# Kernel optimization log

Measured on AMD Instinct MI355X. Metric: run time of the kernel, lower is better.

Reference implementation:

```python
import jax, jax.numpy as jnp
import numpy as np

B, T, S, M = 512, 256, 32, 4  # groups, timesteps, state dim, measure dim


def setup_inputs() -> dict:
    key = jax.random.key(0)
    k = jax.random.split(key, 7)
    obs = jax.random.normal(k[0], (B, T, M), jnp.float32)
    # stable transition matrix: scaled orthogonal
    A = jax.random.normal(k[1], (S, S), jnp.float32)
    F = (0.95 * jnp.linalg.qr(A)[0]).astype(jnp.float32)
    # PSD process noise
    Aq = jax.random.normal(k[2], (S, S), jnp.float32)
    Q = (0.05 * (Aq @ Aq.T) / S + 0.01 * jnp.eye(S)).astype(jnp.float32)
    H = (jax.random.normal(k[3], (M, S), jnp.float32) / jnp.sqrt(S)).astype(jnp.float32)
    # PSD measurement noise
    Ar = jax.random.normal(k[4], (M, M), jnp.float32)
    R = ((Ar @ Ar.T) / M + 0.1 * jnp.eye(M)).astype(jnp.float32)
    init_mean = jax.random.normal(k[5], (B, S), jnp.float32)
    Ai = jax.random.normal(k[6], (B, S, S), jnp.float32)
    init_cov = (jnp.einsum('bij,bkj->bik', Ai, Ai) / S + 0.1 * jnp.eye(S)).astype(jnp.float32)
    return {'input': obs, 'F': F, 'Q': Q, 'H': H, 'R': R,
            'init_mean': init_mean, 'init_cov': init_cov}


def reference(input, F, Q, H, R, init_mean, init_cov):
    """One-step-ahead Kalman filter predictions.
    Returns (meas_means [T,B,M], meas_covs [T,B,M,M])."""

    def step(carry, y):
        m, P = carry  # m: [B,S], P: [B,S,S]
        # --- update with observation y (time t-1) ---
        PHt = jnp.einsum('bij,mj->bim', P, H)                    # [B,S,M]
        Smeas = jnp.einsum('ms,bsn->bmn', H, PHt) + R            # [B,M,M]
        # K = P H^T S^{-1}  (S symmetric)
        K = jnp.swapaxes(jnp.linalg.solve(Smeas, jnp.swapaxes(PHt, -1, -2)), -1, -2)  # [B,S,M]
        resid = y - m @ H.T                                      # [B,M]
        m_u = m + jnp.einsum('bsm,bm->bs', K, resid)
        # (I - K H) P ; note H P = PHt^T since P symmetric
        P_u = P - jnp.einsum('bsm,bim->bsi', K, PHt)
        # --- predict ---
        m_p = m_u @ F.T
        P_p = jnp.einsum('ij,bjk,lk->bil', F, P_u, F) + Q
        # --- measurement distribution ---
        mm = m_p @ H.T                                           # [B,M]
        mc = jnp.einsum('ms,bsi,ni->bmn', H, P_p, H) + R         # [B,M,M]
        return (m_p, P_p), (mm, mc)

    # t = 0: measurement of the initial state prediction
    mm0 = init_mean @ H.T
    mc0 = jnp.einsum('ms,bsi,ni->bmn', H, init_cov, H) + R
    obs_tm1 = jnp.swapaxes(input[:, :-1, :], 0, 1)               # [T-1,B,M]
    _, (mms, mcs) = jax.lax.scan(step, (init_mean, init_cov), obs_tm1)
    meas_means = jnp.concatenate([mm0[None], mms], axis=0)       # [T,B,M]
    meas_covs = jnp.concatenate([mc0[None], mcs], axis=0)        # [T,B,M,M]
    return meas_means, meas_covs
```

## Files before the change

kernel.cpp:

```cpp
#include <hip/hip_runtime.h>

#define BB 512
#define TT 256

typedef __attribute__((ext_vector_type(8)))  short bf8;
typedef __attribute__((ext_vector_type(4)))  short bf4;
typedef __attribute__((ext_vector_type(16))) float f16v;
typedef __attribute__((ext_vector_type(4)))  float f4v;

#define MFMA(a,b,c) __builtin_amdgcn_mfma_f32_32x32x16_bf16((a),(b),(c),0,0,0)

static __device__ __forceinline__ unsigned short f2bf_rne(float x) {
    unsigned u = __builtin_bit_cast(unsigned, x);
    return (unsigned short)((u + 0x7FFFu + ((u >> 16) & 1u)) >> 16);
}
static __device__ __forceinline__ float bf2f(unsigned short h) {
    unsigned u = ((unsigned)h) << 16;
    return __builtin_bit_cast(float, u);
}
static __device__ __forceinline__ void tsplit(float x, short& hi, short& lo) {
    unsigned u = __builtin_bit_cast(unsigned, x);
    hi = (short)(u >> 16);
    float hf = __builtin_bit_cast(float, u & 0xFFFF0000u);
    float l  = x - hf;
    lo = (short)(__builtin_bit_cast(unsigned, l) >> 16);
}
static __device__ __forceinline__ bf8 ld8(const unsigned short* p) {
    bf4 a = *(const bf4*)p;
    bf4 b = *(const bf4*)(p + 4);
    bf8 r;
    r[0]=a[0]; r[1]=a[1]; r[2]=a[2]; r[3]=a[3];
    r[4]=b[0]; r[5]=b[1]; r[6]=b[2]; r[7]=b[3];
    return r;
}

__global__ __launch_bounds__(64)
void kalman_v5(const float* __restrict__ obs,
               const float* __restrict__ Fg,
               const float* __restrict__ Qg,
               const float* __restrict__ Hg,
               const float* __restrict__ Rg,
               const float* __restrict__ im,
               const float* __restrict__ ic,
               float* __restrict__ out)
{
    __shared__ __align__(16) unsigned short sT1h[32*36], sT1l[32*36];
    __shared__ __align__(16) unsigned short sPNh[4*36],  sPNl[4*36];
    __shared__ __align__(16) float sFH[36*40];
    __shared__ __align__(16) float sm[32];
    __shared__ __align__(16) float sS[16];
    __shared__ __align__(16) float sRes4[4];

    const int lane = threadIdx.x;
    const int b    = blockIdx.x;
    const int c    = lane & 31;
    const int h    = lane >> 5;

    bf8 Fh[2], Fl[2], Hh[2], Hl[2];
    #pragma unroll
    for (int kk = 0; kk < 2; ++kk) {
        #pragma unroll
        for (int j = 0; j < 8; ++j) {
            int k = kk*16 + h*8 + j;
            float f = Fg[c*32 + k];
            unsigned short fh = f2bf_rne(f);
            Fh[kk][j] = (short)fh;
            Fl[kk][j] = (short)f2bf_rne(f - bf2f(fh));
            float hv = (c < 4) ? Hg[c*32 + k] : 0.f;
            unsigned short hh = f2bf_rne(hv);
            Hh[kk][j] = (short)hh;
            Hl[kk][j] = (short)f2bf_rne(hv - bf2f(hh));
        }
    }

    f16v Qc, P;
    #pragma unroll
    for (int reg = 0; reg < 16; ++reg) {
        int row = (reg & 3) + 8*(reg >> 2) + 4*h;
        Qc[reg] = Qg[row*32 + c];
        P[reg]  = ic[(size_t)b*1024 + row*32 + c];
    }
    float Rc[4] = {0.f, 0.f, 0.f, 0.f};
    if (c < 4) {
        #pragma unroll
        for (int m = 0; m < 4; ++m) Rc[m] = Rg[m*4 + c];
    }

    #pragma unroll
    for (int e = lane; e < 1024; e += 64) sFH[(e >> 5)*40 + (e & 31)] = Fg[e];
    #pragma unroll
    for (int e = lane; e < 128; e += 64) sFH[(32 + (e >> 5))*40 + (e & 31)] = Hg[e];
    if (lane < 32) sm[lane] = im[b*32 + lane];

    const float* dotrow = &sFH[(lane < 32 ? lane : (32 + (lane & 3))) * 40];
    const bool yl = (lane >= 32 && lane < 36);
    const float* obsp = obs + (size_t)b*TT*4 + (yl ? (lane - 32) : 0);
    float* om = out;
    float* oc = out + (size_t)TT * BB * 4;

    float yv = yl ? obsp[0] : 0.f;

    for (int t = 0; t < TT; ++t) {
        float yv_nxt = (yl && t + 1 < TT) ? obsp[(t + 1) * 4] : 0.f;

        float dotv = 0.f;
        #pragma unroll
        for (int q = 0; q < 8; ++q) {
            f4v a = *(const f4v*)&dotrow[4*q];
            f4v mv = *(const f4v*)&sm[4*q];
            dotv += a.x*mv.x + a.y*mv.y + a.z*mv.z + a.w*mv.w;
        }

        float p2[16];
        #pragma unroll
        for (int r = 0; r < 16; ++r) p2[r] = __shfl_xor(P[r], 32, 64);
        float fr[2][8];
        #pragma unroll
        for (int j = 0; j < 4; ++j) {
            fr[0][j]   = h ? p2[4+j]  : P[j];
            fr[0][4+j] = h ? P[4+j]   : p2[j];
            fr[1][j]   = h ? p2[12+j] : P[8+j];
            fr[1][4+j] = h ? P[12+j]  : p2[8+j];
        }
        bf8 Ph[2], Pl[2];
        #pragma unroll
        for (int kk = 0; kk < 2; ++kk)
            #pragma unroll
            for (int j = 0; j < 8; ++j) {
                short hi, lo;
                tsplit(fr[kk][j], hi, lo);
                Ph[kk][j] = hi;
                Pl[kk][j] = lo;
            }

        f16v tA = 0.0f, tB = 0.0f;
        tA = MFMA(Ph[0], Fh[0], tA);  tB = MFMA(Ph[1], Fh[1], tB);
        tA = MFMA(Ph[0], Fl[0], tA);  tB = MFMA(Ph[1], Fl[1], tB);
        tA = MFMA(Pl[0], Fh[0], tA);  tB = MFMA(Pl[1], Fh[1], tB);

        f16v aA = 0.0f, aB = 0.0f;
        aA = MFMA(Hh[0], Ph[0], aA);  aB = MFMA(Hh[1], Ph[1], aB);
        aA = MFMA(Hh[0], Pl[0], aA);  aB = MFMA(Hh[1], Pl[1], aB);
        aA = MFMA(Hl[0], Ph[0], aA);  aB = MFMA(Hl[1], Ph[1], aB);

        if (lane < 32) {
            #pragma unroll
            for (int n = 0; n < 4; ++n) {
                short hi, lo;
                tsplit(aA[n] + aB[n], hi, lo);
                sPNh[n*36 + c] = (unsigned short)hi;
                sPNl[n*36 + c] = (unsigned short)lo;
            }
        }
        {
            f16v Tp = tA + tB;
            #pragma unroll
            for (int q = 0; q < 4; ++q) {
                int r0 = 8*q + 4*h;
                bf4 vh, vl;
                #pragma unroll
                for (int i = 0; i < 4; ++i) {
                    short hi, lo;
                    tsplit(Tp[4*q + i], hi, lo);
                    vh[i] = hi; vl[i] = lo;
                }
                *(bf4*)&sT1h[c*36 + r0] = vh;
                *(bf4*)&sT1l[c*36 + r0] = vl;
            }
        }

        bf8 N0h, N1h, N0l, N1l;
        if (c < 4) {
            N0h = ld8(&sPNh[c*36 + 8*h]);
            N1h = ld8(&sPNh[c*36 + 16 + 8*h]);
            N0l = ld8(&sPNl[c*36 + 8*h]);
            N1l = ld8(&sPNl[c*36 + 16 + 8*h]);
        } else {
            N0h = (bf8)(short)0; N1h = (bf8)(short)0;
            N0l = (bf8)(short)0; N1l = (bf8)(short)0;
        }
        bf8 T0h = ld8(&sT1h[c*36 + 8*h]);
        bf8 T1h_ = ld8(&sT1h[c*36 + 16 + 8*h]);
        bf8 T0l = ld8(&sT1l[c*36 + 8*h]);
        bf8 T1l_ = ld8(&sT1l[c*36 + 16 + 8*h]);

        f16v sA = 0.0f, sB = 0.0f;
        sA = MFMA(Hh[0], N0h, sA);  sB = MFMA(Hh[1], N1h, sB);
        sA = MFMA(Hh[0], N0l, sA);  sB = MFMA(Hh[1], N1l, sB);
        sA = MFMA(Hl[0], N0h, sA);  sB = MFMA(Hl[1], N1h, sB);

        f16v wA = 0.0f, wB = 0.0f;
        wA = MFMA(N0h, Fh[0], wA);  wB = MFMA(N1h, Fh[1], wB);
        wA = MFMA(N0h, Fl[0], wA);  wB = MFMA(N1h, Fl[1], wB);
        wA = MFMA(N0l, Fh[0], wA);  wB = MFMA(N1l, Fh[1], wB);

        f16v zA = Qc, zB = 0.0f;
        zA = MFMA(Fh[0], T0h, zA);  zB = MFMA(Fh[1], T1h_, zB);
        zA = MFMA(Fh[0], T0l, zA);  zB = MFMA(Fh[1], T1l_, zB);
        zA = MFMA(Fl[0], T0h, zA);  zB = MFMA(Fl[1], T1h_, zB);

        float Smr[4];
        #pragma unroll
        for (int m = 0; m < 4; ++m) Smr[m] = sA[m] + sB[m] + Rc[m];
        if (lane < 32 && c < 4) {
            #pragma unroll
            for (int m = 0; m < 4; ++m)
                oc[(((size_t)t*BB + b)*4 + m)*4 + c] = Smr[m];
            *(f4v*)&sS[c*4] = (f4v){Smr[0], Smr[1], Smr[2], Smr[3]};
        }
        if (yl) {
            om[((size_t)t*BB + b)*4 + (lane - 32)] = dotv;
            sRes4[lane - 32] = yv - dotv;
        }

        if (t == TT - 1) break;
        yv = yv_nxt;

        f4v q0 = *(const f4v*)&sS[0];
        f4v q1 = *(const f4v*)&sS[4];
        f4v q2 = *(const f4v*)&sS[8];
        f4v q3 = *(const f4v*)&sS[12];
        const float S0=q0.x,  S1=q1.x,  S2=q2.x,  S3=q3.x;
        const float S4=q0.y,  S5=q1.y,  S6=q2.y,  S7=q3.y;
        const float S8=q0.z,  S9=q1.z,  S10=q2.z, S11=q3.z;
        const float S12=q0.w, S13=q1.w, S14=q2.w, S15=q3.w;

        float nG0, nG1, nG2, nG3, W0, W1, W2, W3;
        {
            const float A2323 = S10*S15 - S11*S14;
            const float A1323 = S9 *S15 - S11*S13;
            const float A1223 = S9 *S14 - S10*S13;
            const float A0323 = S8 *S15 - S11*S12;
            const float A0223 = S8 *S14 - S10*S12;
            const float A0123 = S8 *S13 - S9 *S12;
            const float A2313 = S6 *S15 - S7 *S14;
            const float A1313 = S5 *S15 - S7 *S13;
            const float A1213 = S5 *S14 - S6 *S13;
            const float A2312 = S6 *S11 - S7 *S10;
            const float A1312 = S5 *S11 - S7 *S9;
            const float A1212 = S5 *S10 - S6 *S9;
            const float A0313 = S4 *S15 - S7 *S12;
            const float A0213 = S4 *S14 - S6 *S12;
            const float A0312 = S4 *S11 - S7 *S8;
            const float A0212 = S4 *S10 - S6 *S8;
            const float A0113 = S4 *S13 - S5 *S12;
            const float A0112 = S4 *S9  - S5 *S8;

            const float i00 =  (S5*A2323 - S6*A1323 + S7*A1223);
            const float i10 = -(S4*A2323 - S6*A0323 + S7*A0223);
            const float i20 =  (S4*A1323 - S5*A0323 + S7*A0123);
            const float i30 = -(S4*A1223 - S5*A0223 + S6*A0123);
            const float i01 = -(S1*A2323 - S2*A1323 + S3*A1223);
            const float i11 =  (S0*A2323 - S2*A0323 + S3*A0223);
            const float i21 = -(S0*A1323 - S1*A0323 + S3*A0123);
            const float i31 =  (S0*A1223 - S1*A0223 + S2*A0123);
            const float i02 =  (S1*A2313 - S2*A1313 + S3*A1213);
            const float i12 = -(S0*A2313 - S2*A0313 + S3*A0213);
            const float i22 =  (S0*A1313 - S1*A0313 + S3*A0113);
            const float i32 = -(S0*A1213 - S1*A0213 + S2*A0113);
            const float i03 = -(S1*A2312 - S2*A1312 + S3*A1212);
            const float i13 =  (S0*A2312 - S2*A0312 + S3*A0212);
            const float i23 = -(S0*A1312 - S1*A0312 + S3*A0112);
            const float i33 =  (S0*A1212 - S1*A0212 + S2*A0112);

            const float det = S0*i00 + S1*i10 + S2*i20 + S3*i30;
            const float nid = -1.0f / det;

            W0 = wA[0] + wB[0];
            W1 = wA[1] + wB[1];
            W2 = wA[2] + wB[2];
            W3 = wA[3] + wB[3];

            nG0 = nid * (W0*i00 + W1*i10 + W2*i20 + W3*i30);
            nG1 = nid * (W0*i01 + W1*i11 + W2*i21 + W3*i31);
            nG2 = nid * (W0*i02 + W1*i12 + W2*i22 + W3*i32);
            nG3 = nid * (W0*i03 + W1*i13 + W2*i23 + W3*i33);
        }

        bf8 Gh = (bf8)(short)0, Gl = (bf8)(short)0;
        bf8 Wbh = (bf8)(short)0, Wbl = (bf8)(short)0;
        {
            float ng[4] = {nG0, nG1, nG2, nG3};
            float wv[4] = {W0, W1, W2, W3};
            #pragma unroll
            for (int j2 = 0; j2 < 4; ++j2) {
                short hi, lo;
                tsplit(ng[j2], hi, lo);
                Gh[j2] = hi; Gl[j2] = lo;
                tsplit(wv[j2], hi, lo);
                Wbh[j2] = hi; Wbl[j2] = lo;
            }
        }
        f16v Pn = zA + zB;
        Pn = MFMA(Gh, Wbh, Pn);
        Pn = MFMA(Gh, Wbl, Pn);
        Pn = MFMA(Gl, Wbh, Pn);
        P = Pn;

        {
            f4v rv = *(const f4v*)&sRes4[0];
            if (lane < 32)
                sm[lane] = dotv - (nG0*rv.x + nG1*rv.y + nG2*rv.z + nG3*rv.w);
        }
    }
}

extern "C" void kernel_launch(void* const* d_in, const int* in_sizes, int n_in,
                              void* d_out, int out_size, void* d_ws, size_t ws_size,
                              hipStream_t stream) {
    const float* obs       = (const float*)d_in[0];
    const float* F         = (const float*)d_in[1];
    const float* Q         = (const float*)d_in[2];
    const float* H         = (const float*)d_in[3];
    const float* R         = (const float*)d_in[4];
    const float* init_mean = (const float*)d_in[5];
    const float* init_cov  = (const float*)d_in[6];
    float* out = (float*)d_out;

    kalman_v5<<<BB, 64, 0, stream>>>(obs, F, Q, H, R, init_mean, init_cov, out);
}
```

Measured before the change: 540.7 us.

## Process two batch groups per wavefront to interleave independent Kalman chains

Each 64-lane block now runs two independent batch filters, interleaving their MFMA chains and scalar gain computations so one chain's latency can hide behind the other's. It also replaces the LDS round trip for the F·P intermediate with a register shuffle transpose. The grid is halved to 256 blocks, which lowers wave-level parallelism across CUs and raises register pressure per wave.

```diff
diff --git a/kernel.cpp b/kernel.cpp
--- a/kernel.cpp
+++ b/kernel.cpp
@@ -34,8 +34,86 @@
     return r;
 }
 
-__global__ __launch_bounds__(64)
-void kalman_v5(const float* __restrict__ obs,
+static __device__ __forceinline__ void mk_bfrag(const f16v M, int h, bf8 Bh[2], bf8 Bl[2]) {
+    float p2[16];
+    #pragma unroll
+    for (int r = 0; r < 16; ++r) p2[r] = __shfl_xor(M[r], 32, 64);
+    float fr[2][8];
+    #pragma unroll
+    for (int j = 0; j < 4; ++j) {
+        fr[0][j]   = h ? p2[4+j]  : M[j];
+        fr[0][4+j] = h ? M[4+j]   : p2[j];
+        fr[1][j]   = h ? p2[12+j] : M[8+j];
+        fr[1][4+j] = h ? M[12+j]  : p2[8+j];
+    }
+    #pragma unroll
+    for (int kk = 0; kk < 2; ++kk)
+        #pragma unroll
+        for (int j = 0; j < 8; ++j) {
+            short hi, lo;
+            tsplit(fr[kk][j], hi, lo);
+            Bh[kk][j] = hi;
+            Bl[kk][j] = lo;
+        }
+}
+
+static __device__ __forceinline__ void gain4(const float* sSp, const float W[4], float nG[4]) {
+    f4v q0 = *(const f4v*)&sSp[0];
+    f4v q1 = *(const f4v*)&sSp[4];
+    f4v q2 = *(const f4v*)&sSp[8];
+    f4v q3 = *(const f4v*)&sSp[12];
+    const float S0=q0.x,  S1=q1.x,  S2=q2.x,  S3=q3.x;
+    const float S4=q0.y,  S5=q1.y,  S6=q2.y,  S7=q3.y;
+    const float S8=q0.z,  S9=q1.z,  S10=q2.z, S11=q3.z;
+    const float S12=q0.w, S13=q1.w, S14=q2.w, S15=q3.w;
+
+    const float A2323 = S10*S15 - S11*S14;
+    const float A1323 = S9 *S15 - S11*S13;
+    const float A1223 = S9 *S14 - S10*S13;
+    const float A0323 = S8 *S15 - S11*S12;
+    const float A0223 = S8 *S14 - S10*S12;
+    const float A0123 = S8 *S13 - S9 *S12;
+    const float A2313 = S6 *S15 - S7 *S14;
+    const float A1313 = S5 *S15 - S7 *S13;
+    const float A1213 = S5 *S14 - S6 *S13;
+    const float A2312 = S6 *S11 - S7 *S10;
+    const float A1312 = S5 *S11 - S7 *S9;
+    const float A1212 = S5 *S10 - S6 *S9;
+    const float A0313 = S4 *S15 - S7 *S12;
+    const float A0213 = S4 *S14 - S6 *S12;
+    const float A0312 = S4 *S11 - S7 *S8;
+    const float A0212 = S4 *S10 - S6 *S8;
+    const float A0113 = S4 *S13 - S5 *S12;
+    const float A0112 = S4 *S9  - S5 *S8;
+
+    const float i00 =  (S5*A2323 - S6*A1323 + S7*A1223);
+    const float i10 = -(S4*A2323 - S6*A0323 + S7*A0223);
+    const float i20 =  (S4*A1323 - S5*A0323 + S7*A0123);
+    const float i30 = -(S4*A1223 - S5*A0223 + S6*A0123);
+    const float i01 = -(S1*A2323 - S2*A1323 + S3*A1223);
+    const float i11 =  (S0*A2323 - S2*A0323 + S3*A0223);
+    const float i21 = -(S0*A1323 - S1*A0323 + S3*A0123);
+    const float i31 =  (S0*A1223 - S1*A0223 + S2*A0123);
+    const float i02 =  (S1*A2313 - S2*A1313 + S3*A1213);
+    const float i12 = -(S0*A2313 - S2*A0313 + S3*A0213);
+    const float i22 =  (S0*A1313 - S1*A0313 + S3*A0113);
+    const float i32 = -(S0*A1213 - S1*A0213 + S2*A0113);
+    const float i03 = -(S1*A2312 - S2*A1312 + S3*A1212);
+    const float i13 =  (S0*A2312 - S2*A0312 + S3*A0212);
+    const float i23 = -(S0*A1312 - S1*A0312 + S3*A0112);
+    const float i33 =  (S0*A1212 - S1*A0212 + S2*A0112);
+
+    const float det = S0*i00 + S1*i10 + S2*i20 + S3*i30;
+    const float nid = -1.0f / det;
+
+    nG[0] = nid * (W[0]*i00 + W[1]*i10 + W[2]*i20 + W[3]*i30);
+    nG[1] = nid * (W[0]*i01 + W[1]*i11 + W[2]*i21 + W[3]*i31);
+    nG[2] = nid * (W[0]*i02 + W[1]*i12 + W[2]*i22 + W[3]*i32);
+    nG[3] = nid * (W[0]*i03 + W[1]*i13 + W[2]*i23 + W[3]*i33);
+}
+
+__global__ __launch_bounds__(64, 1)
+void kalman_v6(const float* __restrict__ obs,
                const float* __restrict__ Fg,
                const float* __restrict__ Qg,
                const float* __restrict__ Hg,
@@ -44,17 +122,16 @@
                const float* __restrict__ ic,
                float* __restrict__ out)
 {
-    __shared__ __align__(16) unsigned short sT1h[32*36], sT1l[32*36];
-    __shared__ __align__(16) unsigned short sPNh[4*36],  sPNl[4*36];
     __shared__ __align__(16) float sFH[36*40];
-    __shared__ __align__(16) float sm[32];
-    __shared__ __align__(16) float sS[16];
-    __shared__ __align__(16) float sRes4[4];
+    __shared__ __align__(16) unsigned short sPNh[2][4*36], sPNl[2][4*36];
+    __shared__ __align__(16) float sS[2][16];
+    __shared__ __align__(16) float sRes[2][4];
+    __shared__ __align__(16) float smv[2][32];
 
     const int lane = threadIdx.x;
-    const int b    = blockIdx.x;
     const int c    = lane & 31;
     const int h    = lane >> 5;
+    const int b0   = blockIdx.x * 2, b1 = b0 + 1;
 
     bf8 Fh[2], Fl[2], Hh[2], Hl[2];
     #pragma unroll
@@ -73,12 +150,13 @@
         }
     }
 
-    f16v Qc, P;
+    f16v Qc, P0, P1;
     #pragma unroll
     for (int reg = 0; reg < 16; ++reg) {
         int row = (reg & 3) + 8*(reg >> 2) + 4*h;
         Qc[reg] = Qg[row*32 + c];
-        P[reg]  = ic[(size_t)b*1024 + row*32 + c];
+        P0[reg] = ic[(size_t)b0*1024 + row*32 + c];
+        P1[reg] = ic[(size_t)b1*1024 + row*32 + c];
     }
     float Rc[4] = {0.f, 0.f, 0.f, 0.f};
     if (c < 4) {
@@ -90,217 +168,181 @@
     for (int e = lane; e < 1024; e += 64) sFH[(e >> 5)*40 + (e & 31)] = Fg[e];
     #pragma unroll
     for (int e = lane; e < 128; e += 64) sFH[(32 + (e >> 5))*40 + (e & 31)] = Hg[e];
-    if (lane < 32) sm[lane] = im[b*32 + lane];
+    if (lane < 32) {
+        smv[0][lane] = im[b0*32 + lane];
+        smv[1][lane] = im[b1*32 + lane];
+    }
 
     const float* dotrow = &sFH[(lane < 32 ? lane : (32 + (lane & 3))) * 40];
     const bool yl = (lane >= 32 && lane < 36);
-    const float* obsp = obs + (size_t)b*TT*4 + (yl ? (lane - 32) : 0);
+    const float* op0 = obs + (size_t)b0*TT*4 + (yl ? (lane - 32) : 0);
+    const float* op1 = obs + (size_t)b1*TT*4 + (yl ? (lane - 32) : 0);
     float* om = out;
     float* oc = out + (size_t)TT * BB * 4;
 
-    float yv = yl ? obsp[0] : 0.f;
+    float y0 = yl ? op0[0] : 0.f;
+    float y1 = yl ? op1[0] : 0.f;
 
     for (int t = 0; t < TT; ++t) {
-        float yv_nxt = (yl && t + 1 < TT) ? obsp[(t + 1) * 4] : 0.f;
-
-        float dotv = 0.f;
+        float y0n = (yl && t + 1 < TT) ? op0[(t + 1) * 4] : 0.f;
+        float y1n = (yl && t + 1 < TT) ? op1[(t + 1) * 4] : 0.f;
+
+        float dot0 = 0.f, dot1 = 0.f;
         #pragma unroll
         for (int q = 0; q < 8; ++q) {
-            f4v a = *(const f4v*)&dotrow[4*q];
-            f4v mv = *(const f4v*)&sm[4*q];
-            dotv += a.x*mv.x + a.y*mv.y + a.z*mv.z + a.w*mv.w;
-        }
-
-        float p2[16];
-        #pragma unroll
-        for (int r = 0; r < 16; ++r) p2[r] = __shfl_xor(P[r], 32, 64);
-        float fr[2][8];
-        #pragma unroll
-        for (int j = 0; j < 4; ++j) {
-            fr[0][j]   = h ? p2[4+j]  : P[j];
-            fr[0][4+j] = h ? P[4+j]   : p2[j];
-            fr[1][j]   = h ? p2[12+j] : P[8+j];
-            fr[1][4+j] = h ? P[12+j]  : p2[8+j];
-        }
-        bf8 Ph[2], Pl[2];
-        #pragma unroll
-        for (int kk = 0; kk < 2; ++kk)
-            #pragma unroll
-            for (int j = 0; j < 8; ++j) {
-                short hi, lo;
-                tsplit(fr[kk][j], hi, lo);
-                Ph[kk][j] = hi;
-                Pl[kk][j] = lo;
-            }
-
-        f16v tA = 0.0f, tB = 0.0f;
-        tA = MFMA(Ph[0], Fh[0], tA);  tB = MFMA(Ph[1], Fh[1], tB);
-        tA = MFMA(Ph[0], Fl[0], tA);  tB = MFMA(Ph[1], Fl[1], tB);
-        tA = MFMA(Pl[0], Fh[0], tA);  tB = MFMA(Pl[1], Fh[1], tB);
-
-        f16v aA = 0.0f, aB = 0.0f;
-        aA = MFMA(Hh[0], Ph[0], aA);  aB = MFMA(Hh[1], Ph[1], aB);
-        aA = MFMA(Hh[0], Pl[0], aA);  aB = MFMA(Hh[1], Pl[1], aB);
-        aA = MFMA(Hl[0], Ph[0], aA);  aB = MFMA(Hl[1], Ph[1], aB);
+            f4v a  = *(const f4v*)&dotrow[4*q];
+            f4v m0 = *(const f4v*)&smv[0][4*q];
+            f4v m1 = *(const f4v*)&smv[1][4*q];
+            dot0 += a.x*m0.x + a.y*m0.y + a.z*m0.z + a.w*m0.w;
+            dot1 += a.x*m1.x + a.y*m1.y + a.z*m1.z + a.w*m1.w;
+        }
+
+        bf8 Ph[2], Pl[2], Qh[2], Ql[2];
+        mk_bfrag(P0, h, Ph, Pl);
+        mk_bfrag(P1, h, Qh, Ql);
+
+        f16v t0A=0.0f, t0B=0.0f, a0A=0.0f, a0B=0.0f;
+        t0A=MFMA(Ph[0],Fh[0],t0A);  t0B=MFMA(Ph[1],Fh[1],t0B);
+        t0A=MFMA(Ph[0],Fl[0],t0A);  t0B=MFMA(Ph[1],Fl[1],t0B);
+        t0A=MFMA(Pl[0],Fh[0],t0A);  t0B=MFMA(Pl[1],Fh[1],t0B);
+        a0A=MFMA(Hh[0],Ph[0],a0A);  a0B=MFMA(Hh[1],Ph[1],a0B);
+        a0A=MFMA(Hh[0],Pl[0],a0A);  a0B=MFMA(Hh[1],Pl[1],a0B);
+        a0A=MFMA(Hl[0],Ph[0],a0A);  a0B=MFMA(Hl[1],Ph[1],a0B);
+
+        f16v t1A=0.0f, t1B=0.0f, a1A=0.0f, a1B=0.0f;
+        t1A=MFMA(Qh[0],Fh[0],t1A);  t1B=MFMA(Qh[1],Fh[1],t1B);
+        t1A=MFMA(Qh[0],Fl[0],t1A);  t1B=MFMA(Qh[1],Fl[1],t1B);
+        t1A=MFMA(Ql[0],Fh[0],t1A);  t1B=MFMA(Ql[1],Fh[1],t1B);
+        a1A=MFMA(Hh[0],Qh[0],a1A);  a1B=MFMA(Hh[1],Qh[1],a1B);
+        a1A=MFMA(Hh[0],Ql[0],a1A);  a1B=MFMA(Hh[1],Ql[1],a1B);
+        a1A=MFMA(Hl[0],Qh[0],a1A);  a1B=MFMA(Hl[1],Qh[1],a1B);
 
         if (lane < 32) {
             #pragma unroll
             for (int n = 0; n < 4; ++n) {
                 short hi, lo;
-                tsplit(aA[n] + aB[n], hi, lo);
-                sPNh[n*36 + c] = (unsigned short)hi;
-                sPNl[n*36 + c] = (unsigned short)lo;
-            }
-        }
+                tsplit(a0A[n] + a0B[n], hi, lo);
+                sPNh[0][n*36 + c] = (unsigned short)hi;
+                sPNl[0][n*36 + c] = (unsigned short)lo;
+                tsplit(a1A[n] + a1B[n], hi, lo);
+                sPNh[1][n*36 + c] = (unsigned short)hi;
+                sPNl[1][n*36 + c] = (unsigned short)lo;
+            }
+        }
+
+        f16v Tp0 = t0A + t0B, Tp1 = t1A + t1B;
+        bf8 T0h[2], T0l[2], T1h[2], T1l[2];
+        mk_bfrag(Tp0, h, T0h, T0l);
+        mk_bfrag(Tp1, h, T1h, T1l);
+
+        bf8 N0h[2], N0l[2], N1h[2], N1l[2];
+        if (c < 4) {
+            N0h[0] = ld8(&sPNh[0][c*36 + 8*h]);
+            N0h[1] = ld8(&sPNh[0][c*36 + 16 + 8*h]);
+            N0l[0] = ld8(&sPNl[0][c*36 + 8*h]);
+            N0l[1] = ld8(&sPNl[0][c*36 + 16 + 8*h]);
+            N1h[0] = ld8(&sPNh[1][c*36 + 8*h]);
+            N1h[1] = ld8(&sPNh[1][c*36 + 16 + 8*h]);
+            N1l[0] = ld8(&sPNl[1][c*36 + 8*h]);
+            N1l[1] = ld8(&sPNl[1][c*36 + 16 + 8*h]);
+        } else {
+            #pragma unroll
+            for (int kk = 0; kk < 2; ++kk) {
+                N0h[kk] = (bf8)(short)0; N0l[kk] = (bf8)(short)0;
+                N1h[kk] = (bf8)(short)0; N1l[kk] = (bf8)(short)0;
+            }
+        }
+
+        f16v s0A=0.0f, s0B=0.0f, w0A=0.0f, w0B=0.0f, z0A=Qc, z0B=0.0f;
+        s0A=MFMA(Hh[0],N0h[0],s0A);  s0B=MFMA(Hh[1],N0h[1],s0B);
+        s0A=MFMA(Hh[0],N0l[0],s0A);  s0B=MFMA(Hh[1],N0l[1],s0B);
+        s0A=MFMA(Hl[0],N0h[0],s0A);  s0B=MFMA(Hl[1],N0h[1],s0B);
+        w0A=MFMA(N0h[0],Fh[0],w0A);  w0B=MFMA(N0h[1],Fh[1],w0B);
+        w0A=MFMA(N0h[0],Fl[0],w0A);  w0B=MFMA(N0h[1],Fl[1],w0B);
+        w0A=MFMA(N0l[0],Fh[0],w0A);  w0B=MFMA(N0l[1],Fh[1],w0B);
+        z0A=MFMA(Fh[0],T0h[0],z0A);  z0B=MFMA(Fh[1],T0h[1],z0B);
+        z0A=MFMA(Fh[0],T0l[0],z0A);  z0B=MFMA(Fh[1],T0l[1],z0B);
+        z0A=MFMA(Fl[0],T0h[0],z0A);  z0B=MFMA(Fl[1],T0h[1],z0B);
+
+        f16v s1A=0.0f, s1B=0.0f, w1A=0.0f, w1B=0.0f, z1A=Qc, z1B=0.0f;
+        s1A=MFMA(Hh[0],N1h[0],s1A);  s1B=MFMA(Hh[1],N1h[1],s1B);
+        s1A=MFMA(Hh[0],N1l[0],s1A);  s1B=MFMA(Hh[1],N1l[1],s1B);
+        s1A=MFMA(Hl[0],N1h[0],s1A);  s1B=MFMA(Hl[1],N1h[1],s1B);
+        w1A=MFMA(N1h[0],Fh[0],w1A);  w1B=MFMA(N1h[1],Fh[1],w1B);
+        w1A=MFMA(N1h[0],Fl[0],w1A);  w1B=MFMA(N1h[1],Fl[1],w1B);
+        w1A=MFMA(N1l[0],Fh[0],w1A);  w1B=MFMA(N1l[1],Fh[1],w1B);
+        z1A=MFMA(Fh[0],T1h[0],z1A);  z1B=MFMA(Fh[1],T1h[1],z1B);
+        z1A=MFMA(Fh[0],T1l[0],z1A);  z1B=MFMA(Fh[1],T1l[1],z1B);
+        z1A=MFMA(Fl[0],T1h[0],z1A);  z1B=MFMA(Fl[1],T1h[1],z1B);
+
+        float Sm0[4], Sm1[4];
+        #pragma unroll
+        for (int m = 0; m < 4; ++m) {
+            Sm0[m] = s0A[m] + s0B[m] + Rc[m];
+            Sm1[m] = s1A[m] + s1B[m] + Rc[m];
+        }
+        if (lane < 32 && c < 4) {
+            #pragma unroll
+            for (int m = 0; m < 4; ++m) {
+                oc[(((size_t)t*BB + b0)*4 + m)*4 + c] = Sm0[m];
+                oc[(((size_t)t*BB + b1)*4 + m)*4 + c] = Sm1[m];
+            }
+            *(f4v*)&sS[0][c*4] = (f4v){Sm0[0], Sm0[1], Sm0[2], Sm0[3]};
+            *(f4v*)&sS[1][c*4] = (f4v){Sm1[0], Sm1[1], Sm1[2], Sm1[3]};
+        }
+        if (yl) {
+            om[((size_t)t*BB + b0)*4 + (lane - 32)] = dot0;
+            om[((size_t)t*BB + b1)*4 + (lane - 32)] = dot1;
+            sRes[0][lane - 32] = y0 - dot0;
+            sRes[1][lane - 32] = y1 - dot1;
+        }
+
+        if (t == TT - 1) break;
+        y0 = y0n; y1 = y1n;
+
         {
-            f16v Tp = tA + tB;
-            #pragma unroll
-            for (int q = 0; q < 4; ++q) {
-                int r0 = 8*q + 4*h;
-                bf4 vh, vl;
-                #pragma unroll
-                for (int i = 0; i < 4; ++i) {
-                    short hi, lo;
-                    tsplit(Tp[4*q + i], hi, lo);
-                    vh[i] = hi; vl[i] = lo;
-                }
-                *(bf4*)&sT1h[c*36 + r0] = vh;
-                *(bf4*)&sT1l[c*36 + r0] = vl;
-            }
-        }
-
-        bf8 N0h, N1h, N0l, N1l;
-        if (c < 4) {
-            N0h = ld8(&sPNh[c*36 + 8*h]);
-            N1h = ld8(&sPNh[c*36 + 16 + 8*h]);
-            N0l = ld8(&sPNl[c*36 + 8*h]);
-            N1l = ld8(&sPNl[c*36 + 16 + 8*h]);
-        } else {
-            N0h = (bf8)(short)0; N1h = (bf8)(short)0;
-            N0l = (bf8)(short)0; N1l = (bf8)(short)0;
-        }
-        bf8 T0h = ld8(&sT1h[c*36 + 8*h]);
-        bf8 T1h_ = ld8(&sT1h[c*36 + 16 + 8*h]);
-        bf8 T0l = ld8(&sT1l[c*36 + 8*h]);
-        bf8 T1l_ = ld8(&sT1l[c*36 + 16 + 8*h]);
-
-        f16v sA = 0.0f, sB = 0.0f;
-        sA = MFMA(Hh[0], N0h, sA);  sB = MFMA(Hh[1], N1h, sB);
-        sA = MFMA(Hh[0], N0l, sA);  sB = MFMA(Hh[1], N1l, sB);
-        sA = MFMA(Hl[0], N0h, sA);  sB = MFMA(Hl[1], N1h, sB);
-
-        f16v wA = 0.0f, wB = 0.0f;
-        wA = MFMA(N0h, Fh[0], wA);  wB = MFMA(N1h, Fh[1], wB);
-        wA = MFMA(N0h, Fl[0], wA);  wB = MFMA(N1h, Fl[1], wB);
-        wA = MFMA(N0l, Fh[0], wA);  wB = MFMA(N1l, Fh[1], wB);
-
-        f16v zA = Qc, zB = 0.0f;
-        zA = MFMA(Fh[0], T0h, zA);  zB = MFMA(Fh[1], T1h_, zB);
-        zA = MFMA(Fh[0], T0l, zA);  zB = MFMA(Fh[1], T1l_, zB);
-        zA = MFMA(Fl[0], T0h, zA);  zB = MFMA(Fl[1], T1h_, zB);
-
-        float Smr[4];
-        #pragma unroll
-        for (int m = 0; m < 4; ++m) Smr[m] = sA[m] + sB[m] + Rc[m];
-        if (lane < 32 && c < 4) {
-            #pragma unroll
-            for (int m = 0; m < 4; ++m)
-                oc[(((size_t)t*BB + b)*4 + m)*4 + c] = Smr[m];
-            *(f4v*)&sS[c*4] = (f4v){Smr[0], Smr[1], Smr[2], Smr[3]};
-        }
-        if (yl) {
-            om[((size_t)t*BB + b)*4 + (lane - 32)] = dotv;
-            sRes4[lane - 32] = yv - dotv;
-        }
-
-        if (t == TT - 1) break;
-        yv = yv_nxt;
-
-        f4v q0 = *(const f4v*)&sS[0];
-        f4v q1 = *(const f4v*)&sS[4];
-        f4v q2 = *(const f4v*)&sS[8];
-        f4v q3 = *(const f4v*)&sS[12];
-        const float S0=q0.x,  S1=q1.x,  S2=q2.x,  S3=q3.x;
-        const float S4=q0.y,  S5=q1.y,  S6=q2.y,  S7=q3.y;
-        const float S8=q0.z,  S9=q1.z,  S10=q2.z, S11=q3.z;
-        const float S12=q0.w, S13=q1.w, S14=q2.w, S15=q3.w;
-
-        float nG0, nG1, nG2, nG3, W0, W1, W2, W3;
+            float W[4] = {w0A[0]+w0B[0], w0A[1]+w0B[1], w0A[2]+w0B[2], w0A[3]+w0B[3]};
+            float nG[4];
+            gain4(&sS[0][0], W, nG);
+
+            bf8 Gh=(bf8)(short)0, Gl=(bf8)(short)0, Wbh=(bf8)(short)0, Wbl=(bf8)(short)0;
+            #pragma unroll
+            for (int j = 0; j < 4; ++j) {
+                short hi, lo;
+                tsplit(nG[j], hi, lo);  Gh[j]=hi;  Gl[j]=lo;
+                tsplit(W[j],  hi, lo);  Wbh[j]=hi; Wbl[j]=lo;
+            }
+            f16v Pn = z0A + z0B;
+            Pn = MFMA(Gh, Wbh, Pn);
+            Pn = MFMA(Gh, Wbl, Pn);
+            Pn = MFMA(Gl, Wbh, Pn);
+            P0 = Pn;
+
+            f4v rv = *(const f4v*)&sRes[0][0];
+            if (lane < 32)
+                smv[0][lane] = dot0 - (nG[0]*rv.x + nG[1]*rv.y + nG[2]*rv.z + nG[3]*rv.w);
+        }
         {
-            const float A2323 = S10*S15 - S11*S14;
-            const float A1323 = S9 *S15 - S11*S13;
-            const float A1223 = S9 *S14 - S10*S13;
-            const float A0323 = S8 *S15 - S11*S12;
-            const float A0223 = S8 *S14 - S10*S12;
-            const float A0123 = S8 *S13 - S9 *S12;
-            const float A2313 = S6 *S15 - S7 *S14;
-            const float A1313 = S5 *S15 - S7 *S13;
-            const float A1213 = S5 *S14 - S6 *S13;
-            const float A2312 = S6 *S11 - S7 *S10;
-            const float A1312 = S5 *S11 - S7 *S9;
-            const float A1212 = S5 *S10 - S6 *S9;
-            const float A0313 = S4 *S15 - S7 *S12;
-            const float A0213 = S4 *S14 - S6 *S12;
-            const float A0312 = S4 *S11 - S7 *S8;
-            const float A0212 = S4 *S10 - S6 *S8;
-            const float A0113 = S4 *S13 - S5 *S12;
-            const float A0112 = S4 *S9  - S5 *S8;
-
-            const float i00 =  (S5*A2323 - S6*A1323 + S7*A1223);
-            const float i10 = -(S4*A2323 - S6*A0323 + S7*A0223);
-            const float i20 =  (S4*A1323 - S5*A0323 + S7*A0123);
-            const float i30 = -(S4*A1223 - S5*A0223 + S6*A0123);
-            const float i01 = -(S1*A2323 - S2*A1323 + S3*A1223);
-            const float i11 =  (S0*A2323 - S2*A0323 + S3*A0223);
-            const float i21 = -(S0*A1323 - S1*A0323 + S3*A0123);
-            const float i31 =  (S0*A1223 - S1*A0223 + S2*A0123);
-            const float i02 =  (S1*A2313 - S2*A1313 + S3*A1213);
-            const float i12 = -(S0*A2313 - S2*A0313 + S3*A0213);
-            const float i22 =  (S0*A1313 - S1*A0313 + S3*A0113);
-            const float i32 = -(S0*A1213 - S1*A0213 + S2*A0113);
-            const float i03 = -(S1*A2312 - S2*A1312 + S3*A1212);
-            const float i13 =  (S0*A2312 - S2*A0312 + S3*A0212);
-            const float i23 = -(S0*A1312 - S1*A0312 + S3*A0112);
-            const float i33 =  (S0*A1212 - S1*A0212 + S2*A0112);
-
-            const float det = S0*i00 + S1*i10 + S2*i20 + S3*i30;
-            const float nid = -1.0f / det;
-
-            W0 = wA[0] + wB[0];
-            W1 = wA[1] + wB[1];
-            W2 = wA[2] + wB[2];
-            W3 = wA[3] + wB[3];
-
-            nG0 = nid * (W0*i00 + W1*i10 + W2*i20 + W3*i30);
-            nG1 = nid * (W0*i01 + W1*i11 + W2*i21 + W3*i31);
-            nG2 = nid * (W0*i02 + W1*i12 + W2*i22 + W3*i32);
-            nG3 = nid * (W0*i03 + W1*i13 + W2*i23 + W3*i33);
-        }
-
-        bf8 Gh = (bf8)(short)0, Gl = (bf8)(short)0;
-        bf8 Wbh = (bf8)(short)0, Wbl = (bf8)(short)0;
-        {
-            float ng[4] = {nG0, nG1, nG2, nG3};
-            float wv[4] = {W0, W1, W2, W3};
-            #pragma unroll
-            for (int j2 = 0; j2 < 4; ++j2) {
+            float W[4] = {w1A[0]+w1B[0], w1A[1]+w1B[1], w1A[2]+w1B[2], w1A[3]+w1B[3]};
+            float nG[4];
+            gain4(&sS[1][0], W, nG);
+
+            bf8 Gh=(bf8)(short)0, Gl=(bf8)(short)0, Wbh=(bf8)(short)0, Wbl=(bf8)(short)0;
+            #pragma unroll
+            for (int j = 0; j < 4; ++j) {
                 short hi, lo;
-                tsplit(ng[j2], hi, lo);
-                Gh[j2] = hi; Gl[j2] = lo;
-                tsplit(wv[j2], hi, lo);
-                Wbh[j2] = hi; Wbl[j2] = lo;
-            }
-        }
-        f16v Pn = zA + zB;
-        Pn = MFMA(Gh, Wbh, Pn);
-        Pn = MFMA(Gh, Wbl, Pn);
-        Pn = MFMA(Gl, Wbh, Pn);
-        P = Pn;
-
-        {
-            f4v rv = *(const f4v*)&sRes4[0];
+                tsplit(nG[j], hi, lo);  Gh[j]=hi;  Gl[j]=lo;
+                tsplit(W[j],  hi, lo);  Wbh[j]=hi; Wbl[j]=lo;
+            }
+            f16v Pn = z1A + z1B;
+            Pn = MFMA(Gh, Wbh, Pn);
+            Pn = MFMA(Gh, Wbl, Pn);
+            Pn = MFMA(Gl, Wbh, Pn);
+            P1 = Pn;
+
+            f4v rv = *(const f4v*)&sRes[1][0];
             if (lane < 32)
-                sm[lane] = dotv - (nG0*rv.x + nG1*rv.y + nG2*rv.z + nG3*rv.w);
+                smv[1][lane] = dot1 - (nG[0]*rv.x + nG[1]*rv.y + nG[2]*rv.z + nG[3]*rv.w);
         }
     }
 }
@@ -317,5 +359,5 @@
     const float* init_cov  = (const float*)d_in[6];
     float* out = (float*)d_out;
 
-    kalman_v5<<<BB, 64, 0, stream>>>(obs, F, Q, H, R, init_mean, init_cov, out);
-}
+    kalman_v6<<<BB/2, 64, 0, stream>>>(obs, F, Q, H, R, init_mean, init_cov, out);
+}
```

New measurement: 934.9 us. 1.73x slower.
